# Optimization experiments

Hardware: AMD Instinct MI355X
Metric: run time of the kernel (lower is better)

## Reference

```python
import jax, jax.numpy as jnp
import numpy as np

DIMS = 2048
SEQ = 4096
INIT_STD = 0.01


def setup_inputs() -> dict:
    key = jax.random.key(0)
    k_in, k_wi, k_wh, k_b = jax.random.split(key, 4)
    inputs = jax.random.normal(k_in, (SEQ, DIMS), dtype=jnp.float32)
    W_hi = jax.random.normal(k_wi, (DIMS, DIMS), dtype=jnp.float32) * INIT_STD
    W_hh = jax.random.normal(k_wh, (DIMS, DIMS), dtype=jnp.float32) * INIT_STD
    b = jax.random.normal(k_b, (DIMS,), dtype=jnp.float32) * INIT_STD
    h0 = jnp.zeros((DIMS,), dtype=jnp.float32)
    return {"inputs": inputs, "W_hi": W_hi, "W_hh": W_hh, "b": b, "h0": h0}


def reference(inputs, W_hi, W_hh, b, h0):
    # bmv(W, x) == x @ W.T for vector x
    def step(h_prev, x):
        h_cur = jnp.tanh(x @ W_hi.T + h_prev @ W_hh.T + b)
        out = x + h_cur  # residual
        return h_cur, out

    _, outputs = jax.lax.scan(step, h0, inputs)  # outputs: [SEQ, DIMS]
    return outputs
```

## Files before the change

kernel.cpp:

```cpp
#include <hip/hip_runtime.h>
#include <hip/hip_bf16.h>
#include <stdint.h>

#define DIMS 2048
#define SEQ  4096
#define NBLK 256
#define RPB  8
#define NW   1024

typedef unsigned long long ull;
typedef unsigned int v4u __attribute__((ext_vector_type(4)));

__device__ __forceinline__ unsigned pk_bf16(float a, float b) {
  unsigned ua = __float_as_uint(a);
  ua += 0x7fffu + ((ua >> 16) & 1u);
  unsigned ub = __float_as_uint(b);
  ub += 0x7fffu + ((ub >> 16) & 1u);
  return (ua >> 16) | (ub & 0xffff0000u);
}
__device__ __forceinline__ float bflo(unsigned u) { return __uint_as_float(u << 16); }
__device__ __forceinline__ float bfhi(unsigned u) { return __uint_as_float(u & 0xffff0000u); }

__global__ __launch_bounds__(256) void gemm_z(const float* __restrict__ X,
                                              const float* __restrict__ W,
                                              const float* __restrict__ bias,
                                              float* __restrict__ Z) {
  __shared__ float xs[64][33];
  __shared__ float ws[64][33];
  const int tid = threadIdx.x;
  const int tx = tid & 15;
  const int ty = tid >> 4;
  const int s0 = blockIdx.x * 64;
  const int d0 = blockIdx.y * 64;

  float acc[4][4] = {};

  for (int k0 = 0; k0 < DIMS; k0 += 32) {
#pragma unroll
    for (int i = 0; i < 2; ++i) {
      int idx = tid + i * 256;
      int r = idx >> 3;
      int c = (idx & 7) << 2;
      float4 xv = *(const float4*)&X[(size_t)(s0 + r) * DIMS + k0 + c];
      xs[r][c] = xv.x; xs[r][c + 1] = xv.y; xs[r][c + 2] = xv.z; xs[r][c + 3] = xv.w;
      float4 wv = *(const float4*)&W[(size_t)(d0 + r) * DIMS + k0 + c];
      ws[r][c] = wv.x; ws[r][c + 1] = wv.y; ws[r][c + 2] = wv.z; ws[r][c + 3] = wv.w;
    }
    __syncthreads();
#pragma unroll
    for (int k = 0; k < 32; ++k) {
      float a_[4], b_[4];
#pragma unroll
      for (int i = 0; i < 4; ++i) a_[i] = xs[ty * 4 + i][k];
#pragma unroll
      for (int j = 0; j < 4; ++j) b_[j] = ws[tx * 4 + j][k];
#pragma unroll
      for (int i = 0; i < 4; ++i)
#pragma unroll
        for (int j = 0; j < 4; ++j) acc[i][j] += a_[i] * b_[j];
    }
    __syncthreads();
  }

  const float4 bv = *(const float4*)&bias[d0 + tx * 4];
#pragma unroll
  for (int i = 0; i < 4; ++i) {
    float4 o;
    o.x = acc[i][0] + bv.x; o.y = acc[i][1] + bv.y;
    o.z = acc[i][2] + bv.z; o.w = acc[i][3] + bv.w;
    *(float4*)&Z[(size_t)(s0 + ty * 4 + i) * DIMS + d0 + tx * 4] = o;
  }
}

__global__ __launch_bounds__(256) void rnn_seq(const float* __restrict__ X,
                                               const float* __restrict__ Whh,
                                               const float* __restrict__ h0,
                                               float* __restrict__ ZO,
                                               ull* __restrict__ hb2)
{
  __shared__ uint4 hsb[2][DIMS / 8];

  const int tid = threadIdx.x;
  const int b   = blockIdx.x;
  const int r   = tid >> 5;
  const int c   = tid & 31;
  const int grow = b * RPB + r;

  uint4 wq[8];
  {
    const float* wrow = Whh + (size_t)grow * DIMS + c * 64;
#pragma unroll
    for (int m = 0; m < 8; ++m) {
      float4 a = *(const float4*)(wrow + m * 8);
      float4 d = *(const float4*)(wrow + m * 8 + 4);
      wq[m] = make_uint4(pk_bf16(a.x, a.y), pk_bf16(a.z, a.w),
                         pk_bf16(d.x, d.y), pk_bf16(d.z, d.w));
    }
  }

  if (tid < 4) {
    unsigned pair = pk_bf16(h0[b * RPB + 2 * tid], h0[b * RPB + 2 * tid + 1]);
    __hip_atomic_store(&hb2[NW + b * 4 + tid], (ull)pair,
                       __ATOMIC_RELAXED, __HIP_MEMORY_SCOPE_AGENT);
  }
  float zpre = 0.f, xpre = 0.f;
  if (c == 0) { zpre = ZO[grow]; xpre = X[grow]; }

  for (int t = 0; t < SEQ; ++t) {
    const ull* src = hb2 + (size_t)((t + 1) & 1) * NW + tid * 4;
    const unsigned want = (unsigned)t;
    v4u p01, p23;
    do {
      asm volatile(
          "global_load_dwordx4 %0, %2, off sc0 sc1\n\t"
          "global_load_dwordx4 %1, %3, off sc0 sc1\n\t"
          "s_waitcnt vmcnt(0)"
          : "=&v"(p01), "=&v"(p23)
          : "v"(src), "v"(src + 2)
          : "memory");
    } while (p01.y != want || p01.w != want || p23.y != want || p23.w != want);

    {
      const int c0 = tid >> 3, m0 = tid & 7;
      hsb[t & 1][c0 * 8 + (m0 ^ (c0 & 7))] = make_uint4(p01.x, p01.z, p23.x, p23.z);
    }
    __syncthreads();

    float acc = 0.f;
#pragma unroll
    for (int m = 0; m < 8; ++m) {
      uint4 w = wq[m];
      uint4 h = hsb[t & 1][c * 8 + (m ^ (c & 7))];
      acc += bflo(w.x) * bflo(h.x) + bfhi(w.x) * bfhi(h.x);
      acc += bflo(w.y) * bflo(h.y) + bfhi(w.y) * bfhi(h.y);
      acc += bflo(w.z) * bflo(h.z) + bfhi(w.z) * bfhi(h.z);
      acc += bflo(w.w) * bflo(h.w) + bfhi(w.w) * bfhi(h.w);
    }
#pragma unroll
    for (int off = 16; off > 0; off >>= 1) acc += __shfl_xor(acc, off);

    float hcur = 0.f;
    if (c == 0) hcur = tanhf(acc + zpre);
    float hhi = __shfl(hcur, 32);
    if ((tid & 63) == 0) {
      ull pk = ((ull)(unsigned)(t + 1) << 32) | (ull)pk_bf16(hcur, hhi);
      __hip_atomic_store(&hb2[(size_t)(t & 1) * NW + b * 4 + (tid >> 6)], pk,
                         __ATOMIC_RELAXED, __HIP_MEMORY_SCOPE_AGENT);
    }

    if (c == 0) {
      ZO[(size_t)t * DIMS + grow] = xpre + hcur;
      if (t + 1 < SEQ) {
        zpre = ZO[(size_t)(t + 1) * DIMS + grow];
        xpre = X[(size_t)(t + 1) * DIMS + grow];
      }
    }
  }
}

extern "C" void kernel_launch(void* const* d_in, const int* in_sizes, int n_in,
                              void* d_out, int out_size, void* d_ws, size_t ws_size,
                              hipStream_t stream) {
  (void)in_sizes; (void)n_in; (void)out_size; (void)ws_size;
  const float* X    = (const float*)d_in[0];
  const float* Whi  = (const float*)d_in[1];
  const float* Whh  = (const float*)d_in[2];
  const float* bias = (const float*)d_in[3];
  const float* h0   = (const float*)d_in[4];
  float* out = (float*)d_out;

  ull* hb2 = (ull*)d_ws;

  hipMemsetAsync(hb2, 0xFF, 2 * NW * sizeof(ull), stream);

  dim3 g(SEQ / 64, DIMS / 64);
  gemm_z<<<g, 256, 0, stream>>>(X, Whi, bias, out);
  rnn_seq<<<NBLK, 256, 0, stream>>>(X, Whh, h0, out, hb2);
}
```

Measured before the change: 8.073 ms.

## Batch per-step Z/X loads and output stores into 16-step LDS chunks

The recurrent kernel used to do a scalar global load of the precomputed Z and X values and a scalar output store on every timestep, and those sat on the serial critical path. Now every 16 steps a few threads bulk-load Z and X into shared memory as float4 and flush the buffered outputs from the previous chunk. The inner step loop then only touches LDS for these values, taking global-memory latency off the per-step chain. The cost is an extra pair of block barriers per chunk and a small amount of shared memory.

```diff
diff --git a/kernel.cpp b/kernel.cpp
--- a/kernel.cpp
+++ b/kernel.cpp
@@ -7,6 +7,7 @@
 #define NBLK 256
 #define RPB  8
 #define NW   1024
+#define CHUNK 16
 
 typedef unsigned long long ull;
 typedef unsigned int v4u __attribute__((ext_vector_type(4)));
@@ -79,12 +80,16 @@
                                                ull* __restrict__ hb2)
 {
   __shared__ uint4 hsb[2][DIMS / 8];
+  __shared__ float zbuf[CHUNK][RPB];
+  __shared__ float xbuf[CHUNK][RPB];
+  __shared__ float obuf[CHUNK][RPB];
 
   const int tid = threadIdx.x;
   const int b   = blockIdx.x;
   const int r   = tid >> 5;
   const int c   = tid & 31;
-  const int grow = b * RPB + r;
+  const int brow = b * RPB;
+  const int grow = brow + r;
 
   uint4 wq[8];
   {
@@ -99,62 +104,86 @@
   }
 
   if (tid < 4) {
-    unsigned pair = pk_bf16(h0[b * RPB + 2 * tid], h0[b * RPB + 2 * tid + 1]);
+    unsigned pair = pk_bf16(h0[brow + 2 * tid], h0[brow + 2 * tid + 1]);
     __hip_atomic_store(&hb2[NW + b * 4 + tid], (ull)pair,
                        __ATOMIC_RELAXED, __HIP_MEMORY_SCOPE_AGENT);
   }
-  float zpre = 0.f, xpre = 0.f;
-  if (c == 0) { zpre = ZO[grow]; xpre = X[grow]; }
-
-  for (int t = 0; t < SEQ; ++t) {
-    const ull* src = hb2 + (size_t)((t + 1) & 1) * NW + tid * 4;
-    const unsigned want = (unsigned)t;
-    v4u p01, p23;
-    do {
-      asm volatile(
-          "global_load_dwordx4 %0, %2, off sc0 sc1\n\t"
-          "global_load_dwordx4 %1, %3, off sc0 sc1\n\t"
-          "s_waitcnt vmcnt(0)"
-          : "=&v"(p01), "=&v"(p23)
-          : "v"(src), "v"(src + 2)
-          : "memory");
-    } while (p01.y != want || p01.w != want || p23.y != want || p23.w != want);
-
-    {
-      const int c0 = tid >> 3, m0 = tid & 7;
-      hsb[t & 1][c0 * 8 + (m0 ^ (c0 & 7))] = make_uint4(p01.x, p01.z, p23.x, p23.z);
-    }
-    __syncthreads();
-
-    float acc = 0.f;
-#pragma unroll
-    for (int m = 0; m < 8; ++m) {
-      uint4 w = wq[m];
-      uint4 h = hsb[t & 1][c * 8 + (m ^ (c & 7))];
-      acc += bflo(w.x) * bflo(h.x) + bfhi(w.x) * bfhi(h.x);
-      acc += bflo(w.y) * bflo(h.y) + bfhi(w.y) * bfhi(h.y);
-      acc += bflo(w.z) * bflo(h.z) + bfhi(w.z) * bfhi(h.z);
-      acc += bflo(w.w) * bflo(h.w) + bfhi(w.w) * bfhi(h.w);
-    }
-#pragma unroll
-    for (int off = 16; off > 0; off >>= 1) acc += __shfl_xor(acc, off);
-
-    float hcur = 0.f;
-    if (c == 0) hcur = tanhf(acc + zpre);
-    float hhi = __shfl(hcur, 32);
-    if ((tid & 63) == 0) {
-      ull pk = ((ull)(unsigned)(t + 1) << 32) | (ull)pk_bf16(hcur, hhi);
-      __hip_atomic_store(&hb2[(size_t)(t & 1) * NW + b * 4 + (tid >> 6)], pk,
-                         __ATOMIC_RELAXED, __HIP_MEMORY_SCOPE_AGENT);
-    }
-
-    if (c == 0) {
-      ZO[(size_t)t * DIMS + grow] = xpre + hcur;
-      if (t + 1 < SEQ) {
-        zpre = ZO[(size_t)(t + 1) * DIMS + grow];
-        xpre = X[(size_t)(t + 1) * DIMS + grow];
-      }
-    }
+
+  for (int T = 0; T < SEQ; T += CHUNK) {
+    __syncthreads();
+    if (tid < 32) {
+      if (T > 0) {
+        int s = tid >> 1, col = (tid & 1) * 4;
+        *(float4*)&ZO[(size_t)(T - CHUNK + s) * DIMS + brow + col] =
+            *(float4*)&obuf[s][col];
+      }
+    } else if (tid < 64) {
+      int q = tid - 32, s = q >> 1, col = (q & 1) * 4;
+      *(float4*)&zbuf[s][col] =
+          *(const float4*)&ZO[(size_t)(T + s) * DIMS + brow + col];
+    } else if (tid < 96) {
+      int q = tid - 64, s = q >> 1, col = (q & 1) * 4;
+      *(float4*)&xbuf[s][col] =
+          *(const float4*)&X[(size_t)(T + s) * DIMS + brow + col];
+    }
+    __syncthreads();
+
+    for (int s = 0; s < CHUNK; ++s) {
+      const int t = T + s;
+
+      const ull* src = hb2 + (size_t)((t + 1) & 1) * NW + tid * 4;
+      const unsigned want = (unsigned)t;
+      v4u p01, p23;
+      do {
+        asm volatile(
+            "global_load_dwordx4 %0, %2, off sc0 sc1\n\t"
+            "global_load_dwordx4 %1, %3, off sc0 sc1\n\t"
+            "s_waitcnt vmcnt(0)"
+            : "=&v"(p01), "=&v"(p23)
+            : "v"(src), "v"(src + 2)
+            : "memory");
+      } while (p01.y != want || p01.w != want || p23.y != want || p23.w != want);
+
+      {
+        const int c0 = tid >> 3, m0 = tid & 7;
+        hsb[t & 1][c0 * 8 + (m0 ^ (c0 & 7))] =
+            make_uint4(p01.x, p01.z, p23.x, p23.z);
+      }
+      __syncthreads();
+
+      float zcur = 0.f, xcur = 0.f;
+      if (c == 0) { zcur = zbuf[s][r]; xcur = xbuf[s][r]; }
+
+      float acc = 0.f;
+#pragma unroll
+      for (int m = 0; m < 8; ++m) {
+        uint4 w = wq[m];
+        uint4 h = hsb[t & 1][c * 8 + (m ^ (c & 7))];
+        acc += bflo(w.x) * bflo(h.x) + bfhi(w.x) * bfhi(h.x);
+        acc += bflo(w.y) * bflo(h.y) + bfhi(w.y) * bfhi(h.y);
+        acc += bflo(w.z) * bflo(h.z) + bfhi(w.z) * bfhi(h.z);
+        acc += bflo(w.w) * bflo(h.w) + bfhi(w.w) * bfhi(h.w);
+      }
+#pragma unroll
+      for (int off = 16; off > 0; off >>= 1) acc += __shfl_xor(acc, off);
+
+      float hcur = 0.f;
+      if (c == 0) hcur = tanhf(acc + zcur);
+      float hhi = __shfl(hcur, 32);
+      if ((tid & 63) == 0) {
+        ull pk = ((ull)(unsigned)(t + 1) << 32) | (ull)pk_bf16(hcur, hhi);
+        __hip_atomic_store(&hb2[(size_t)(t & 1) * NW + b * 4 + (tid >> 6)], pk,
+                           __ATOMIC_RELAXED, __HIP_MEMORY_SCOPE_AGENT);
+      }
+      if (c == 0) obuf[s][r] = xcur + hcur;
+    }
+  }
+
+  __syncthreads();
+  if (tid < 32) {
+    int s = tid >> 1, col = (tid & 1) * 4;
+    *(float4*)&ZO[(size_t)(SEQ - CHUNK + s) * DIMS + brow + col] =
+        *(float4*)&obuf[s][col];
   }
 }
 
```

New measurement: 17.75 ms. 120% more time.

## Compute recurrent matvec directly from polled h registers, dropping LDS h staging

Applied to the files above, without the earlier changes.

Each thread now owns an 8-column slice of all 8 rows instead of one row's 64-column slice. The h values it polls from global memory are therefore exactly the columns it multiplies, so the shared-memory staging of h is removed. The dot products are reduced with a transpose-style shuffle pattern and a small cross-wave LDS sum, and the final tanh, publish and output write are handled by 8 threads of wave 0. This shortens the per-step critical path by removing the LDS broadcast, at the cost of more shuffles and a serialized tail on a few lanes.

```diff
diff --git a/kernel.cpp b/kernel.cpp
--- a/kernel.cpp
+++ b/kernel.cpp
@@ -78,33 +78,31 @@
                                                float* __restrict__ ZO,
                                                ull* __restrict__ hb2)
 {
-  __shared__ uint4 hsb[2][DIMS / 8];
+  __shared__ float wsum[2][4][RPB];
 
-  const int tid = threadIdx.x;
-  const int b   = blockIdx.x;
-  const int r   = tid >> 5;
-  const int c   = tid & 31;
-  const int grow = b * RPB + r;
+  const int tid  = threadIdx.x;
+  const int b    = blockIdx.x;
+  const int lane = tid & 63;
+  const int w    = tid >> 6;
+  const int brow = b * RPB;
 
   uint4 wq[8];
-  {
-    const float* wrow = Whh + (size_t)grow * DIMS + c * 64;
 #pragma unroll
-    for (int m = 0; m < 8; ++m) {
-      float4 a = *(const float4*)(wrow + m * 8);
-      float4 d = *(const float4*)(wrow + m * 8 + 4);
-      wq[m] = make_uint4(pk_bf16(a.x, a.y), pk_bf16(a.z, a.w),
-                         pk_bf16(d.x, d.y), pk_bf16(d.z, d.w));
-    }
+  for (int r = 0; r < RPB; ++r) {
+    const float* wrow = Whh + (size_t)(brow + r) * DIMS + tid * 8;
+    float4 a = *(const float4*)wrow;
+    float4 d = *(const float4*)(wrow + 4);
+    wq[r] = make_uint4(pk_bf16(a.x, a.y), pk_bf16(a.z, a.w),
+                       pk_bf16(d.x, d.y), pk_bf16(d.z, d.w));
   }
 
   if (tid < 4) {
-    unsigned pair = pk_bf16(h0[b * RPB + 2 * tid], h0[b * RPB + 2 * tid + 1]);
+    unsigned pair = pk_bf16(h0[brow + 2 * tid], h0[brow + 2 * tid + 1]);
     __hip_atomic_store(&hb2[NW + b * 4 + tid], (ull)pair,
                        __ATOMIC_RELAXED, __HIP_MEMORY_SCOPE_AGENT);
   }
   float zpre = 0.f, xpre = 0.f;
-  if (c == 0) { zpre = ZO[grow]; xpre = X[grow]; }
+  if (tid < RPB) { zpre = ZO[brow + tid]; xpre = X[brow + tid]; }
 
   for (int t = 0; t < SEQ; ++t) {
     const ull* src = hb2 + (size_t)((t + 1) & 1) * NW + tid * 4;
@@ -120,39 +118,57 @@
           : "memory");
     } while (p01.y != want || p01.w != want || p23.y != want || p23.w != want);
 
+    float hf[8];
     {
-      const int c0 = tid >> 3, m0 = tid & 7;
-      hsb[t & 1][c0 * 8 + (m0 ^ (c0 & 7))] = make_uint4(p01.x, p01.z, p23.x, p23.z);
+      unsigned hd0 = p01.x, hd1 = p01.z, hd2 = p23.x, hd3 = p23.z;
+      hf[0] = bflo(hd0); hf[1] = bfhi(hd0);
+      hf[2] = bflo(hd1); hf[3] = bfhi(hd1);
+      hf[4] = bflo(hd2); hf[5] = bfhi(hd2);
+      hf[6] = bflo(hd3); hf[7] = bfhi(hd3);
     }
+    float acc[8];
+#pragma unroll
+    for (int r = 0; r < RPB; ++r) {
+      uint4 q = wq[r];
+      acc[r] = bflo(q.x) * hf[0] + bfhi(q.x) * hf[1]
+             + bflo(q.y) * hf[2] + bfhi(q.y) * hf[3]
+             + bflo(q.z) * hf[4] + bfhi(q.z) * hf[5]
+             + bflo(q.w) * hf[6] + bfhi(q.w) * hf[7];
+    }
+
+#pragma unroll
+    for (int off = 1; off <= 4; off <<= 1)
+#pragma unroll
+      for (int r = 0; r < RPB; ++r) acc[r] += __shfl_xor(acc[r], off);
+    const int rr = lane & 7;
+    float v = acc[0];
+    v = (rr == 1) ? acc[1] : v;
+    v = (rr == 2) ? acc[2] : v;
+    v = (rr == 3) ? acc[3] : v;
+    v = (rr == 4) ? acc[4] : v;
+    v = (rr == 5) ? acc[5] : v;
+    v = (rr == 6) ? acc[6] : v;
+    v = (rr == 7) ? acc[7] : v;
+#pragma unroll
+    for (int off = 8; off <= 32; off <<= 1) v += __shfl_xor(v, off);
+
+    if (lane < RPB) wsum[t & 1][w][lane] = v;
     __syncthreads();
 
-    float acc = 0.f;
-#pragma unroll
-    for (int m = 0; m < 8; ++m) {
-      uint4 w = wq[m];
-      uint4 h = hsb[t & 1][c * 8 + (m ^ (c & 7))];
-      acc += bflo(w.x) * bflo(h.x) + bfhi(w.x) * bfhi(h.x);
-      acc += bflo(w.y) * bflo(h.y) + bfhi(w.y) * bfhi(h.y);
-      acc += bflo(w.z) * bflo(h.z) + bfhi(w.z) * bfhi(h.z);
-      acc += bflo(w.w) * bflo(h.w) + bfhi(w.w) * bfhi(h.w);
-    }
-#pragma unroll
-    for (int off = 16; off > 0; off >>= 1) acc += __shfl_xor(acc, off);
-
-    float hcur = 0.f;
-    if (c == 0) hcur = tanhf(acc + zpre);
-    float hhi = __shfl(hcur, 32);
-    if ((tid & 63) == 0) {
-      ull pk = ((ull)(unsigned)(t + 1) << 32) | (ull)pk_bf16(hcur, hhi);
-      __hip_atomic_store(&hb2[(size_t)(t & 1) * NW + b * 4 + (tid >> 6)], pk,
-                         __ATOMIC_RELAXED, __HIP_MEMORY_SCOPE_AGENT);
-    }
-
-    if (c == 0) {
-      ZO[(size_t)t * DIMS + grow] = xpre + hcur;
+    if (tid < RPB) {
+      float s = wsum[t & 1][0][tid] + wsum[t & 1][1][tid]
+              + wsum[t & 1][2][tid] + wsum[t & 1][3][tid];
+      float hcur = tanhf(s + zpre);
+      float hnxt = __shfl_xor(hcur, 1);
+      if ((tid & 1) == 0) {
+        ull pk = ((ull)(unsigned)(t + 1) << 32) | (ull)pk_bf16(hcur, hnxt);
+        __hip_atomic_store(&hb2[(size_t)(t & 1) * NW + b * 4 + (tid >> 1)], pk,
+                           __ATOMIC_RELAXED, __HIP_MEMORY_SCOPE_AGENT);
+      }
+      ZO[(size_t)t * DIMS + brow + tid] = xpre + hcur;
       if (t + 1 < SEQ) {
-        zpre = ZO[(size_t)(t + 1) * DIMS + grow];
-        xpre = X[(size_t)(t + 1) * DIMS + grow];
+        zpre = ZO[(size_t)(t + 1) * DIMS + brow + tid];
+        xpre = X[(size_t)(t + 1) * DIMS + brow + tid];
       }
     }
   }
```

Result: slower. 10.85 ms (+34.4%).
